# Kernel tuning notes

Hardware: AMD Instinct MI355X
Metric: run time of the kernel (lower is better)

## Reference

```python
import jax, jax.numpy as jnp
import numpy as np

FS = 5  # filter_size


def _extract_patches(x, fs):
    """x: (B, C, H, W) -> (B, C, fs*fs, H, W), 'same' padding, row-major
    shift order matching conv2d with an identity (one-hot) kernel."""
    B, C, H, W = x.shape
    pad = fs // 2
    xp = jnp.pad(x, ((0, 0), (0, 0), (pad, pad), (pad, pad)))
    shifts = [xp[:, :, i:i + H, j:j + W] for i in range(fs) for j in range(fs)]
    return jnp.stack(shifts, axis=2)


def setup_inputs() -> dict:
    key = jax.random.key(0)
    k1, k2 = jax.random.split(key)
    B, C, H, W = 8, 32, 128, 128
    x = jax.random.normal(k1, (B, C, H, W), dtype=jnp.float32)
    # PPDFGen modeled as a per-pixel linear map C -> fs^2 (1x1 conv) + bias
    w_gen = jax.random.normal(k2, (FS * FS, C), dtype=jnp.float32) * (1.0 / np.sqrt(C))
    b_gen = jnp.zeros((FS * FS,), dtype=jnp.float32)
    return {"x": x, "w_gen": w_gen, "b_gen": b_gen}


def reference(x, w_gen, b_gen):
    # Per-pixel dynamic filters: (B, fs^2, H, W)
    filters = jnp.einsum('bchw,fc->bfhw', x, w_gen) + b_gen[None, :, None, None]
    # Shifted patches (im2col via identity-kernel conv in the original):
    patches = _extract_patches(x, FS)            # (B, C, fs^2, H, W)
    # Elementwise multiply by filters (broadcast over channels) and reduce
    # over the fs^2 tap axis -- same math as the per-channel loop + concat.
    out = jnp.einsum('bcfhw,bfhw->bchw', patches, filters)
    return out
```

## Files before the change

### kernel.cpp

```cpp
#include <hip/hip_runtime.h>

#define FS    5
#define NTAP  25
#define Cc    32
#define CG    8
#define Hc    128
#define Wc    128
#define HW    (Hc * Wc)

#define TH      8
#define TW      64
#define HALO_H  12
#define HALO_W  72
#define PLANE   (HALO_H * HALO_W)
#define F4_PER_PLANE (PLANE / 4)
#define F4_TOTAL     (CG * F4_PER_PLANE)
#define LDS_BYTES    (CG * PLANE * 4)

__device__ __attribute__((aligned(16))) float ZERO4[4];

__device__ __forceinline__ void gload_lds16(const float* g, float* lds) {
    __builtin_amdgcn_global_load_lds(
        (const __attribute__((address_space(1))) void*)g,
        (__attribute__((address_space(3))) void*)lds, 16, 0, 0);
}

__global__ __launch_bounds__(256, 3) void ppdfn_fused(
    const float* __restrict__ x, const float* __restrict__ wg,
    const float* __restrict__ bg, float* __restrict__ out)
{
    extern __shared__ float xs[];

    const int tid = threadIdx.x;
    const int bid = blockIdx.x;
    const int ht  = bid & 15;
    const int wt  = (bid >> 4) & 1;
    const int chg = (bid >> 5) & 3;
    const int b   = bid >> 7;
    const int h0  = ht * TH;
    const int w0  = wt * TW;
    const int c0  = chg * CG;

    const float* xb = x  + (size_t)b * Cc * HW;
    const float* xo = xb + (size_t)c0 * HW;

#pragma unroll
    for (int k = 0; k < 7; ++k) {
        const int f = k * 256 + tid;
        if (f < F4_TOTAL) {
            const int c  = f / F4_PER_PLANE;
            const int rm = f - c * F4_PER_PLANE;
            const int r  = rm / 18;
            const int c4 = rm - r * 18;
            const int gh = h0 - 2 + r;
            const int gw = w0 - 4 + 4 * c4;
            const bool v = ((unsigned)gh < (unsigned)Hc) &&
                           ((unsigned)gw <= (unsigned)(Wc - 4));
            const float* src = v ? (xo + (size_t)c * HW + gh * Wc + gw) : ZERO4;
            gload_lds16(src, xs + (size_t)k * 1024 + (size_t)(tid >> 6) * 256);
        }
    }

    const int ty = tid >> 5;
    const int tx = tid & 31;
    const int w2 = tx * 2;
    const int centerOff = (h0 + ty) * Wc + (w0 + w2);

    const int g1 = (c0 + 8)  & 31;
    const int g2 = (c0 + 16) & 31;
    const int g3 = (c0 + 24) & 31;

    float2 cv[32];
    {
        const float* cb = xb + centerOff;
#pragma unroll
        for (int u = 0; u < 8; ++u)
            cv[8 + u] = *reinterpret_cast<const float2*>(cb + (size_t)(g1 + u) * HW);
#pragma unroll
        for (int u = 0; u < 8; ++u)
            cv[16 + u] = *reinterpret_cast<const float2*>(cb + (size_t)(g2 + u) * HW);
#pragma unroll
        for (int u = 0; u < 8; ++u)
            cv[24 + u] = *reinterpret_cast<const float2*>(cb + (size_t)(g3 + u) * HW);
    }

    float fx[NTAP], fy[NTAP];
#pragma unroll
    for (int t = 0; t < NTAP; ++t) { const float bv = bg[t]; fx[t] = bv; fy[t] = bv; }

    asm volatile("s_waitcnt vmcnt(0)" ::: "memory");
    __builtin_amdgcn_sched_barrier(0);
    __builtin_amdgcn_s_barrier();

#pragma unroll
    for (int u = 0; u < 8; ++u)
        cv[u] = *reinterpret_cast<const float2*>(
            xs + u * PLANE + (ty + 2) * HALO_W + (w2 + 4));

#pragma unroll
    for (int t = 0; t < NTAP; ++t) {
        const float* wr = wg + t * Cc;
#pragma unroll
        for (int u = 0; u < 8; ++u) {
            const float wv = wr[c0 + u];
            fx[t] = fmaf(wv, cv[u].x, fx[t]);
            fy[t] = fmaf(wv, cv[u].y, fy[t]);
        }
#pragma unroll
        for (int u = 0; u < 8; ++u) {
            const float wv = wr[g1 + u];
            fx[t] = fmaf(wv, cv[8 + u].x, fx[t]);
            fy[t] = fmaf(wv, cv[8 + u].y, fy[t]);
        }
#pragma unroll
        for (int u = 0; u < 8; ++u) {
            const float wv = wr[g2 + u];
            fx[t] = fmaf(wv, cv[16 + u].x, fx[t]);
            fy[t] = fmaf(wv, cv[16 + u].y, fy[t]);
        }
#pragma unroll
        for (int u = 0; u < 8; ++u) {
            const float wv = wr[g3 + u];
            fx[t] = fmaf(wv, cv[24 + u].x, fx[t]);
            fy[t] = fmaf(wv, cv[24 + u].y, fy[t]);
        }
    }

    float* ob = out + ((size_t)b * Cc + c0) * HW + centerOff;
#pragma unroll
    for (int c = 0; c < CG; ++c) {
        const float* p = xs + c * PLANE + ty * HALO_W + (w2 + 2);
        float ax = 0.f, ay = 0.f;
#pragma unroll
        for (int di = 0; di < FS; ++di) {
            const float* row = p + di * HALO_W;
            const float2 s01 = *reinterpret_cast<const float2*>(row);
            const float2 s23 = *reinterpret_cast<const float2*>(row + 2);
            const float2 s45 = *reinterpret_cast<const float2*>(row + 4);
            const float s0 = s01.x, s1 = s01.y, s2 = s23.x,
                        s3 = s23.y, s4 = s45.x, s5 = s45.y;
            ax = fmaf(fx[di * FS + 0], s0, ax);  ay = fmaf(fy[di * FS + 0], s1, ay);
            ax = fmaf(fx[di * FS + 1], s1, ax);  ay = fmaf(fy[di * FS + 1], s2, ay);
            ax = fmaf(fx[di * FS + 2], s2, ax);  ay = fmaf(fy[di * FS + 2], s3, ay);
            ax = fmaf(fx[di * FS + 3], s3, ax);  ay = fmaf(fy[di * FS + 3], s4, ay);
            ax = fmaf(fx[di * FS + 4], s4, ax);  ay = fmaf(fy[di * FS + 4], s5, ay);
        }
        *reinterpret_cast<float2*>(ob + (size_t)c * HW) = make_float2(ax, ay);
    }
}

extern "C" void kernel_launch(void* const* d_in, const int* in_sizes, int n_in,
                              void* d_out, int out_size, void* d_ws, size_t ws_size,
                              hipStream_t stream) {
    const float* x  = (const float*)d_in[0];
    const float* wg = (const float*)d_in[1];
    const float* bg = (const float*)d_in[2];
    float* out = (float*)d_out;

    ppdfn_fused<<<dim3(1024), 256, LDS_BYTES, stream>>>(x, wg, bg, out);
}
```

Baseline: 26.50 us.

## Split filter generation into separate kernel to remove redundant per-channel-group recompute

The fused kernel recomputed the 25-tap per-pixel filters in each of the four channel-group blocks, reading all 32 channels at the centre pixels each time. The filter generation now runs once in its own kernel that writes the filters to workspace, and the apply kernel reads 25 float2 filter values per thread instead. This removes the fourfold redundant matmul and the register pressure, and raises the occupancy hint to 4. In exchange it adds a second launch and a write plus re-read of a B×25×H×W filter tensor through global memory.

```diff
diff --git a/kernel.cpp b/kernel.cpp
--- a/kernel.cpp
+++ b/kernel.cpp
@@ -25,9 +25,38 @@
         (__attribute__((address_space(3))) void*)lds, 16, 0, 0);
 }
 
-__global__ __launch_bounds__(256, 3) void ppdfn_fused(
+__global__ __launch_bounds__(256) void gen_kernel(
     const float* __restrict__ x, const float* __restrict__ wg,
-    const float* __restrict__ bg, float* __restrict__ out)
+    const float* __restrict__ bg, float* __restrict__ filt)
+{
+    const int p = blockIdx.x * 256 + threadIdx.x;
+    const int b = blockIdx.y;
+
+    const float* xb = x + (size_t)b * Cc * HW + p;
+    float xv[Cc];
+#pragma unroll
+    for (int c = 0; c < Cc; ++c) xv[c] = xb[(size_t)c * HW];
+
+    float f[NTAP];
+#pragma unroll
+    for (int t = 0; t < NTAP; ++t) f[t] = bg[t];
+
+#pragma unroll
+    for (int t = 0; t < NTAP; ++t) {
+        const float* wr = wg + t * Cc;
+#pragma unroll
+        for (int c = 0; c < Cc; ++c)
+            f[t] = fmaf(wr[c], xv[c], f[t]);
+    }
+
+    float* fb = filt + (size_t)b * NTAP * HW + p;
+#pragma unroll
+    for (int t = 0; t < NTAP; ++t) fb[(size_t)t * HW] = f[t];
+}
+
+__global__ __launch_bounds__(256, 4) void apply_kernel(
+    const float* __restrict__ x, const float* __restrict__ filt,
+    float* __restrict__ out)
 {
     extern __shared__ float xs[];
 
@@ -41,8 +70,7 @@
     const int w0  = wt * TW;
     const int c0  = chg * CG;
 
-    const float* xb = x  + (size_t)b * Cc * HW;
-    const float* xo = xb + (size_t)c0 * HW;
+    const float* xo = x + ((size_t)b * Cc + c0) * HW;
 
 #pragma unroll
     for (int k = 0; k < 7; ++k) {
@@ -66,65 +94,15 @@
     const int w2 = tx * 2;
     const int centerOff = (h0 + ty) * Wc + (w0 + w2);
 
-    const int g1 = (c0 + 8)  & 31;
-    const int g2 = (c0 + 16) & 31;
-    const int g3 = (c0 + 24) & 31;
-
-    float2 cv[32];
-    {
-        const float* cb = xb + centerOff;
+    float2 ft[NTAP];
+    const float* fb = filt + (size_t)b * NTAP * HW + centerOff;
 #pragma unroll
-        for (int u = 0; u < 8; ++u)
-            cv[8 + u] = *reinterpret_cast<const float2*>(cb + (size_t)(g1 + u) * HW);
-#pragma unroll
-        for (int u = 0; u < 8; ++u)
-            cv[16 + u] = *reinterpret_cast<const float2*>(cb + (size_t)(g2 + u) * HW);
-#pragma unroll
-        for (int u = 0; u < 8; ++u)
-            cv[24 + u] = *reinterpret_cast<const float2*>(cb + (size_t)(g3 + u) * HW);
-    }
-
-    float fx[NTAP], fy[NTAP];
-#pragma unroll
-    for (int t = 0; t < NTAP; ++t) { const float bv = bg[t]; fx[t] = bv; fy[t] = bv; }
+    for (int t = 0; t < NTAP; ++t)
+        ft[t] = *reinterpret_cast<const float2*>(fb + (size_t)t * HW);
 
     asm volatile("s_waitcnt vmcnt(0)" ::: "memory");
     __builtin_amdgcn_sched_barrier(0);
     __builtin_amdgcn_s_barrier();
-
-#pragma unroll
-    for (int u = 0; u < 8; ++u)
-        cv[u] = *reinterpret_cast<const float2*>(
-            xs + u * PLANE + (ty + 2) * HALO_W + (w2 + 4));
-
-#pragma unroll
-    for (int t = 0; t < NTAP; ++t) {
-        const float* wr = wg + t * Cc;
-#pragma unroll
-        for (int u = 0; u < 8; ++u) {
-            const float wv = wr[c0 + u];
-            fx[t] = fmaf(wv, cv[u].x, fx[t]);
-            fy[t] = fmaf(wv, cv[u].y, fy[t]);
-        }
-#pragma unroll
-        for (int u = 0; u < 8; ++u) {
-            const float wv = wr[g1 + u];
-            fx[t] = fmaf(wv, cv[8 + u].x, fx[t]);
-            fy[t] = fmaf(wv, cv[8 + u].y, fy[t]);
-        }
-#pragma unroll
-        for (int u = 0; u < 8; ++u) {
-            const float wv = wr[g2 + u];
-            fx[t] = fmaf(wv, cv[16 + u].x, fx[t]);
-            fy[t] = fmaf(wv, cv[16 + u].y, fy[t]);
-        }
-#pragma unroll
-        for (int u = 0; u < 8; ++u) {
-            const float wv = wr[g3 + u];
-            fx[t] = fmaf(wv, cv[24 + u].x, fx[t]);
-            fy[t] = fmaf(wv, cv[24 + u].y, fy[t]);
-        }
-    }
 
     float* ob = out + ((size_t)b * Cc + c0) * HW + centerOff;
 #pragma unroll
@@ -139,11 +117,11 @@
             const float2 s45 = *reinterpret_cast<const float2*>(row + 4);
             const float s0 = s01.x, s1 = s01.y, s2 = s23.x,
                         s3 = s23.y, s4 = s45.x, s5 = s45.y;
-            ax = fmaf(fx[di * FS + 0], s0, ax);  ay = fmaf(fy[di * FS + 0], s1, ay);
-            ax = fmaf(fx[di * FS + 1], s1, ax);  ay = fmaf(fy[di * FS + 1], s2, ay);
-            ax = fmaf(fx[di * FS + 2], s2, ax);  ay = fmaf(fy[di * FS + 2], s3, ay);
-            ax = fmaf(fx[di * FS + 3], s3, ax);  ay = fmaf(fy[di * FS + 3], s4, ay);
-            ax = fmaf(fx[di * FS + 4], s4, ax);  ay = fmaf(fy[di * FS + 4], s5, ay);
+            ax = fmaf(ft[di * FS + 0].x, s0, ax);  ay = fmaf(ft[di * FS + 0].y, s1, ay);
+            ax = fmaf(ft[di * FS + 1].x, s1, ax);  ay = fmaf(ft[di * FS + 1].y, s2, ay);
+            ax = fmaf(ft[di * FS + 2].x, s2, ax);  ay = fmaf(ft[di * FS + 2].y, s3, ay);
+            ax = fmaf(ft[di * FS + 3].x, s3, ax);  ay = fmaf(ft[di * FS + 3].y, s4, ay);
+            ax = fmaf(ft[di * FS + 4].x, s4, ax);  ay = fmaf(ft[di * FS + 4].y, s5, ay);
         }
         *reinterpret_cast<float2*>(ob + (size_t)c * HW) = make_float2(ax, ay);
     }
@@ -156,6 +134,8 @@
     const float* wg = (const float*)d_in[1];
     const float* bg = (const float*)d_in[2];
     float* out = (float*)d_out;
+    float* filt = (float*)d_ws;
 
-    ppdfn_fused<<<dim3(1024), 256, LDS_BYTES, stream>>>(x, wg, bg, out);
+    gen_kernel<<<dim3(HW / 256, 8), 256, 0, stream>>>(x, wg, bg, filt);
+    apply_kernel<<<dim3(1024), 256, LDS_BYTES, stream>>>(x, filt, out);
 }
```

Result: slower. 36.57 us (+38.0%).
